# Kernel tuning notes

Measured on AMD Instinct MI355X. Metric: run time of the kernel, lower is better.

## Reference

```python
import jax, jax.numpy as jnp
import numpy as np

B, F, N = 32, 10, 512   # batch_num, win_size (all_feature), node_num
E = 8192                # edges per graph
INTER = 256             # GAT inter_dim
HEADS = 2
NEG_SLOPE = 0.2
BN_EPS = 1e-5


def setup_inputs() -> dict:
    key = jax.random.key(0)
    ks = jax.random.split(key, 16)
    data = jax.random.normal(ks[0], (B, F, N), dtype=jnp.float32)
    # loop-free random edges: src != dst (matches PyG remove_self_loops + add_self_loops)
    dst = jax.random.randint(ks[1], (E,), 0, N)
    off = jax.random.randint(ks[2], (E,), 1, N)
    src = (dst + off) % N
    org_edge_index = jnp.stack([src, dst]).astype(jnp.int64)
    g = 0.05
    return {
        "data": data,
        "org_edge_index": org_edge_index,
        "W1": jax.random.normal(ks[3], (F, HEADS * INTER), dtype=jnp.float32) * g,
        "as1": jax.random.normal(ks[4], (HEADS, INTER), dtype=jnp.float32) * g,
        "ad1": jax.random.normal(ks[5], (HEADS, INTER), dtype=jnp.float32) * g,
        "b1": jnp.zeros((HEADS * INTER,), dtype=jnp.float32),
        "W2": jax.random.normal(ks[6], (HEADS * INTER, HEADS * INTER), dtype=jnp.float32) * g,
        "as2": jax.random.normal(ks[7], (HEADS, INTER), dtype=jnp.float32) * g,
        "ad2": jax.random.normal(ks[8], (HEADS, INTER), dtype=jnp.float32) * g,
        "b2": jnp.zeros((HEADS * INTER,), dtype=jnp.float32),
        "Wfc": jax.random.normal(ks[9], (HEADS * INTER, 1), dtype=jnp.float32) * g,
        "bfc": jnp.zeros((1,), dtype=jnp.float32),
        "gamma": jnp.ones((1,), dtype=jnp.float32),
        "beta": jnp.zeros((1,), dtype=jnp.float32),
    }


def _gat_conv(x, src, dst, W, a_src, a_dst, b):
    # PyG GATConv (v1), concat=True, negative_slope=0.2
    n = x.shape[0]
    H, C = a_src.shape
    h = (x @ W).reshape(n, H, C)                       # [n, H, C]
    al_s = jnp.einsum('nhc,hc->nh', h, a_src)          # [n, H]
    al_d = jnp.einsum('nhc,hc->nh', h, a_dst)
    e = jax.nn.leaky_relu(al_s[src] + al_d[dst], NEG_SLOPE)  # [Etot, H]
    emax = jax.ops.segment_max(e, dst, num_segments=n)       # segment softmax over dst
    ex = jnp.exp(e - emax[dst])
    denom = jax.ops.segment_sum(ex, dst, num_segments=n)
    alpha = ex / (denom[dst] + 1e-16)                  # [Etot, H]
    msg = h[src] * alpha[:, :, None]                   # [Etot, H, C]
    out = jax.ops.segment_sum(msg, dst, num_segments=n)
    return out.reshape(n, H * C) + b


def reference(data, org_edge_index, W1, as1, ad1, b1, W2, as2, ad2, b2,
              Wfc, bfc, gamma, beta):
    b_num, feat, n_num = data.shape
    x = data.reshape(-1, feat)                         # faithful to x.view(-1, all_feature)
    total = b_num * n_num
    # batched edge index: repeat with per-batch node offsets
    offs = jnp.arange(b_num, dtype=org_edge_index.dtype) * n_num
    be = (org_edge_index[:, None, :] + offs[None, :, None]).reshape(2, -1)
    loops = jnp.arange(total, dtype=org_edge_index.dtype)  # add_self_loops
    src = jnp.concatenate([be[0], loops])
    dst = jnp.concatenate([be[1], loops])
    x1 = _gat_conv(x, src, dst, W1, as1, ad1, b1)      # dropout = identity (eval)
    x2 = _gat_conv(x1, src, dst, W2, as2, ad2, b2)
    y = x2 @ Wfc + bfc                                 # [total, 1]
    # BatchNorm1d(1), eval mode: running_mean=0, running_var=1
    y = y * (gamma / jnp.sqrt(1.0 + BN_EPS)) + beta
    y = jax.nn.relu(y)
    return y.reshape(-1, 1, n_num)                     # [B, 1, N]
```

## Files before the change

kernel.cpp:

```cpp
#include <hip/hip_runtime.h>
#include <math.h>

#define B_  32
#define F_  10
#define N_  512
#define E_  8192
#define T_  16384
#define EC_ 8704
#define HC_ 512
#define C_  256

typedef __attribute__((ext_vector_type(8))) short bf16x8;
typedef __attribute__((ext_vector_type(4))) float f32x4;

__device__ __forceinline__ unsigned short f2bf(float f) {
    unsigned int u = __float_as_uint(f);
    u = (u + 0x7fffu + ((u >> 16) & 1u)) >> 16;
    return (unsigned short)u;
}
__device__ __forceinline__ float bf2f(unsigned short b) {
    return __uint_as_float(((unsigned int)b) << 16);
}
__device__ __forceinline__ float dot4(f32x4 a, f32x4 b) {
    f32x4 m = a * b;
    return m[0] + m[1] + m[2] + m[3];
}
__device__ __forceinline__ unsigned int pack2(unsigned short a, unsigned short b) {
    return (unsigned int)a | ((unsigned int)b << 16);
}
__device__ __forceinline__ void bf2x2(unsigned int u, float& f0, float& f1) {
    f0 = __uint_as_float(u << 16);
    f1 = __uint_as_float(u & 0xffff0000u);
}
__device__ __forceinline__ void async_cp16(const void* g, void* l) {
    __builtin_amdgcn_global_load_lds(
        (const __attribute__((address_space(1))) unsigned int*)g,
        (__attribute__((address_space(3))) unsigned int*)l, 16, 0, 0);
}

__device__ __forceinline__ int node_map(int bid, int wid) {
    int x = bid & 7;
    int rest = bid >> 3;
    int batch = x * 4 + (rest >> 7);
    int within = rest & 127;
    return batch * 512 + within * 4 + wid;
}

__global__ __launch_bounds__(256) void gemm1_kernel(
    const float* __restrict__ X, const float* __restrict__ W1,
    const float* __restrict__ a_s, const float* __restrict__ a_d,
    unsigned short* __restrict__ Hs, float* __restrict__ als,
    float* __restrict__ ald, float* __restrict__ als2z,
    float* __restrict__ ald2z,
    const int* __restrict__ eidx, const float* __restrict__ W2,
    int* __restrict__ off0, int* __restrict__ csr0,
    unsigned short* __restrict__ Bhi, unsigned short* __restrict__ Blo) {
    __shared__ float shmem[1056];
    int tid = threadIdx.x;

    if (blockIdx.x >= 512) {
        if (blockIdx.x < 768) {
            int pb = blockIdx.x - 512;
            float* t = shmem;
            int bx = pb & 15, by = pb >> 4;
            int kb = bx * 32, nb = by * 32;
            int tx = tid & 31, ty = tid >> 5;
#pragma unroll
            for (int r = ty; r < 32; r += 8)
                t[r * 33 + tx] = W2[(size_t)(kb + r) * HC_ + nb + tx];
            __syncthreads();
#pragma unroll
            for (int r = ty; r < 32; r += 8) {
                float v = t[tx * 33 + r];
                unsigned short h = f2bf(v);
                Bhi[(size_t)(nb + r) * HC_ + kb + tx] = h;
                Blo[(size_t)(nb + r) * HC_ + kb + tx] = f2bf(v - bf2f(h));
            }
        } else {
            int* cnt = (int*)shmem;
            int* scn = (int*)shmem + 512;
            cnt[2 * tid] = 0; cnt[2 * tid + 1] = 0;
            __syncthreads();
            const int* edst = eidx + E_;
            for (int j = tid; j < EC_; j += 256) {
                int d = (j < E_) ? edst[j] : (j - E_);
                atomicAdd(&cnt[d], 1);
            }
            __syncthreads();
            int c0 = cnt[2 * tid], c1 = cnt[2 * tid + 1];
            scn[tid] = c0 + c1;
            __syncthreads();
            for (int d = 1; d < 256; d <<= 1) {
                int add = (tid >= d) ? scn[tid - d] : 0;
                __syncthreads();
                scn[tid] += add;
                __syncthreads();
            }
            int e0 = scn[tid] - (c0 + c1);
            off0[2 * tid] = e0;
            off0[2 * tid + 1] = e0 + c0;
            cnt[2 * tid] = e0;
            cnt[2 * tid + 1] = e0 + c0;
            if (tid == 255) off0[512] = EC_;
            __syncthreads();
            for (int j = tid; j < EC_; j += 256) {
                int s, d;
                if (j < E_) { s = eidx[j]; d = edst[j]; }
                else { s = d = j - E_; }
                int pos = atomicAdd(&cnt[d], 1);
                csr0[pos] = s;
            }
        }
        return;
    }

    float* xs = shmem;
    int lane = tid & 63, w = tid >> 6;
    int q = blockIdx.x;
    int batch = (q & 7) * 4 + (q >> 7);
    int sub = (q >> 3) & 15;
    int nb = batch * 512 + sub * 32 + w * 8;
    int col = lane * 8;

    f32x4 w1r[F_][2];
#pragma unroll
    for (int k = 0; k < F_; ++k) {
        w1r[k][0] = *(const f32x4*)&W1[k * HC_ + col];
        w1r[k][1] = *(const f32x4*)&W1[k * HC_ + col + 4];
    }
    f32x4 asl = *(const f32x4*)&a_s[col], ash = *(const f32x4*)&a_s[col + 4];
    f32x4 adl = *(const f32x4*)&a_d[col], adh = *(const f32x4*)&a_d[col + 4];

    const float* xp = X + (size_t)nb * F_;
    if (lane < 40) {
        xs[w * 80 + lane] = xp[lane];
        xs[w * 80 + lane + 40] = xp[lane + 40];
    }
    if (lane < 16) als2z[nb * 2 + lane] = 0.f;
    else if (lane >= 48) ald2z[nb * 2 + lane - 48] = 0.f;

#pragma unroll
    for (int n = 0; n < 8; ++n) {
        f32x4 h0 = {0.f, 0.f, 0.f, 0.f}, h1 = h0;
#pragma unroll
        for (int k = 0; k < F_; ++k) {
            float xv = xs[w * 80 + n * F_ + k];
            h0 += xv * w1r[k][0];
            h1 += xv * w1r[k][1];
        }
        int node = nb + n;
        uint4 uh;
        uh.x = pack2(f2bf(h0[0]), f2bf(h0[1]));
        uh.y = pack2(f2bf(h0[2]), f2bf(h0[3]));
        uh.z = pack2(f2bf(h1[0]), f2bf(h1[1]));
        uh.w = pack2(f2bf(h1[2]), f2bf(h1[3]));
        *(uint4*)&Hs[(size_t)node * HC_ + col] = uh;
        float ps = dot4(h0, asl) + dot4(h1, ash);
        float pd = dot4(h0, adl) + dot4(h1, adh);
#pragma unroll
        for (int m = 1; m <= 16; m <<= 1) {
            ps += __shfl_xor(ps, m);
            pd += __shfl_xor(pd, m);
        }
        if (lane == 0)  { als[node * 2 + 0] = ps; ald[node * 2 + 0] = pd; }
        if (lane == 32) { als[node * 2 + 1] = ps; ald[node * 2 + 1] = pd; }
    }
}

template <int MODE>
__global__ __launch_bounds__(256) void agg_kernel(
    const unsigned short* __restrict__ Hin, const float* __restrict__ als,
    const float* __restrict__ ald, const int* __restrict__ off0,
    const int* __restrict__ csr0, const float* __restrict__ bias,
    unsigned short* __restrict__ Ahi,
    const float* __restrict__ Wfc, const float* __restrict__ bfc,
    const float* __restrict__ gamma, const float* __restrict__ beta,
    float* __restrict__ out) {
    int tid = threadIdx.x, lane = tid & 63, wid = tid >> 6;
    int dst = node_map(blockIdx.x, wid);
    int bbase = dst & ~511;
    int dl = dst & 511;
    int beg = off0[dl], end = off0[dl + 1], deg = end - beg;
    float ad0 = ald[2 * dst], ad1 = ald[2 * dst + 1];
    int col = lane * 8;
    float A[8] = {0.f, 0.f, 0.f, 0.f, 0.f, 0.f, 0.f, 0.f};

    if (deg <= 64) {
        float e0 = -1e30f, e1 = -1e30f;
        int sl = 0;
        if (lane < deg) {
            sl = csr0[beg + lane] + bbase;
            float a0 = als[2 * sl], a1 = als[2 * sl + 1];
            e0 = a0 + ad0; e0 = e0 > 0.f ? e0 : 0.2f * e0;
            e1 = a1 + ad1; e1 = e1 > 0.f ? e1 : 0.2f * e1;
        }
        float m0 = e0, m1 = e1;
#pragma unroll
        for (int m = 1; m < 64; m <<= 1) {
            m0 = fmaxf(m0, __shfl_xor(m0, m));
            m1 = fmaxf(m1, __shfl_xor(m1, m));
        }
        float x0 = (lane < deg) ? expf(e0 - m0) : 0.f;
        float x1 = (lane < deg) ? expf(e1 - m1) : 0.f;
        float d0 = x0, d1 = x1;
#pragma unroll
        for (int m = 1; m < 64; m <<= 1) {
            d0 += __shfl_xor(d0, m);
            d1 += __shfl_xor(d1, m);
        }
        float w0l = x0 / (d0 + 1e-16f);
        float w1l = x1 / (d1 + 1e-16f);
        int e = 0;
        for (; e + 4 <= deg; e += 4) {
            int s0 = __shfl(sl, e), s1 = __shfl(sl, e + 1);
            int s2 = __shfl(sl, e + 2), s3 = __shfl(sl, e + 3);
            float wa0 = __shfl(w0l, e),     wb0 = __shfl(w1l, e);
            float wa1 = __shfl(w0l, e + 1), wb1 = __shfl(w1l, e + 1);
            float wa2 = __shfl(w0l, e + 2), wb2 = __shfl(w1l, e + 2);
            float wa3 = __shfl(w0l, e + 3), wb3 = __shfl(w1l, e + 3);
            float w0 = (lane < 32) ? wa0 : wb0;
            float w1 = (lane < 32) ? wa1 : wb1;
            float w2 = (lane < 32) ? wa2 : wb2;
            float w3 = (lane < 32) ? wa3 : wb3;
            uint4 h0 = *(const uint4*)(Hin + (size_t)s0 * HC_ + col);
            uint4 h1 = *(const uint4*)(Hin + (size_t)s1 * HC_ + col);
            uint4 h2 = *(const uint4*)(Hin + (size_t)s2 * HC_ + col);
            uint4 h3 = *(const uint4*)(Hin + (size_t)s3 * HC_ + col);
            float f0, f1;
            bf2x2(h0.x, f0, f1); A[0] = fmaf(w0, f0, A[0]); A[1] = fmaf(w0, f1, A[1]);
            bf2x2(h0.y, f0, f1); A[2] = fmaf(w0, f0, A[2]); A[3] = fmaf(w0, f1, A[3]);
            bf2x2(h0.z, f0, f1); A[4] = fmaf(w0, f0, A[4]); A[5] = fmaf(w0, f1, A[5]);
            bf2x2(h0.w, f0, f1); A[6] = fmaf(w0, f0, A[6]); A[7] = fmaf(w0, f1, A[7]);
            bf2x2(h1.x, f0, f1); A[0] = fmaf(w1, f0, A[0]); A[1] = fmaf(w1, f1, A[1]);
            bf2x2(h1.y, f0, f1); A[2] = fmaf(w1, f0, A[2]); A[3] = fmaf(w1, f1, A[3]);
            bf2x2(h1.z, f0, f1); A[4] = fmaf(w1, f0, A[4]); A[5] = fmaf(w1, f1, A[5]);
            bf2x2(h1.w, f0, f1); A[6] = fmaf(w1, f0, A[6]); A[7] = fmaf(w1, f1, A[7]);
            bf2x2(h2.x, f0, f1); A[0] = fmaf(w2, f0, A[0]); A[1] = fmaf(w2, f1, A[1]);
            bf2x2(h2.y, f0, f1); A[2] = fmaf(w2, f0, A[2]); A[3] = fmaf(w2, f1, A[3]);
            bf2x2(h2.z, f0, f1); A[4] = fmaf(w2, f0, A[4]); A[5] = fmaf(w2, f1, A[5]);
            bf2x2(h2.w, f0, f1); A[6] = fmaf(w2, f0, A[6]); A[7] = fmaf(w2, f1, A[7]);
            bf2x2(h3.x, f0, f1); A[0] = fmaf(w3, f0, A[0]); A[1] = fmaf(w3, f1, A[1]);
            bf2x2(h3.y, f0, f1); A[2] = fmaf(w3, f0, A[2]); A[3] = fmaf(w3, f1, A[3]);
            bf2x2(h3.z, f0, f1); A[4] = fmaf(w3, f0, A[4]); A[5] = fmaf(w3, f1, A[5]);
            bf2x2(h3.w, f0, f1); A[6] = fmaf(w3, f0, A[6]); A[7] = fmaf(w3, f1, A[7]);
        }
        for (; e < deg; ++e) {
            int s = __shfl(sl, e);
            float wa = __shfl(w0l, e);
            float wb = __shfl(w1l, e);
            float w = (lane < 32) ? wa : wb;
            uint4 hv = *(const uint4*)(Hin + (size_t)s * HC_ + col);
            float f0, f1;
            bf2x2(hv.x, f0, f1); A[0] = fmaf(w, f0, A[0]); A[1] = fmaf(w, f1, A[1]);
            bf2x2(hv.y, f0, f1); A[2] = fmaf(w, f0, A[2]); A[3] = fmaf(w, f1, A[3]);
            bf2x2(hv.z, f0, f1); A[4] = fmaf(w, f0, A[4]); A[5] = fmaf(w, f1, A[5]);
            bf2x2(hv.w, f0, f1); A[6] = fmaf(w, f0, A[6]); A[7] = fmaf(w, f1, A[7]);
        }
    } else {
        float m0 = -1e30f, m1 = -1e30f;
        for (int k = beg + lane; k < end; k += 64) {
            int s = csr0[k] + bbase;
            float e0 = als[2 * s] + ad0; e0 = e0 > 0.f ? e0 : 0.2f * e0;
            float e1 = als[2 * s + 1] + ad1; e1 = e1 > 0.f ? e1 : 0.2f * e1;
            m0 = fmaxf(m0, e0);
            m1 = fmaxf(m1, e1);
        }
#pragma unroll
        for (int m = 1; m < 64; m <<= 1) {
            m0 = fmaxf(m0, __shfl_xor(m0, m));
            m1 = fmaxf(m1, __shfl_xor(m1, m));
        }
        float d0 = 0.f, d1 = 0.f;
        for (int k = beg + lane; k < end; k += 64) {
            int s = csr0[k] + bbase;
            float e0 = als[2 * s] + ad0; e0 = e0 > 0.f ? e0 : 0.2f * e0;
            float e1 = als[2 * s + 1] + ad1; e1 = e1 > 0.f ? e1 : 0.2f * e1;
            d0 += expf(e0 - m0);
            d1 += expf(e1 - m1);
        }
#pragma unroll
        for (int m = 1; m < 64; m <<= 1) {
            d0 += __shfl_xor(d0, m);
            d1 += __shfl_xor(d1, m);
        }
        float inv0 = 1.f / (d0 + 1e-16f);
        float inv1 = 1.f / (d1 + 1e-16f);
        for (int k = beg; k < end; ++k) {
            int s = csr0[k] + bbase;
            float e0 = als[2 * s] + ad0; e0 = e0 > 0.f ? e0 : 0.2f * e0;
            float e1 = als[2 * s + 1] + ad1; e1 = e1 > 0.f ? e1 : 0.2f * e1;
            float w0 = expf(e0 - m0) * inv0;
            float w1 = expf(e1 - m1) * inv1;
            float w = (lane < 32) ? w0 : w1;
            uint4 hv = *(const uint4*)(Hin + (size_t)s * HC_ + col);
            float f0, f1;
            bf2x2(hv.x, f0, f1); A[0] = fmaf(w, f0, A[0]); A[1] = fmaf(w, f1, A[1]);
            bf2x2(hv.y, f0, f1); A[2] = fmaf(w, f0, A[2]); A[3] = fmaf(w, f1, A[3]);
            bf2x2(hv.z, f0, f1); A[4] = fmaf(w, f0, A[4]); A[5] = fmaf(w, f1, A[5]);
            bf2x2(hv.w, f0, f1); A[6] = fmaf(w, f0, A[6]); A[7] = fmaf(w, f1, A[7]);
        }
    }

#pragma unroll
    for (int j = 0; j < 8; ++j) A[j] += bias[col + j];

    if (MODE == 0) {
        uint4 uh;
        uh.x = pack2(f2bf(A[0]), f2bf(A[1]));
        uh.y = pack2(f2bf(A[2]), f2bf(A[3]));
        uh.z = pack2(f2bf(A[4]), f2bf(A[5]));
        uh.w = pack2(f2bf(A[6]), f2bf(A[7]));
        *(uint4*)&Ahi[(size_t)dst * HC_ + col] = uh;
    } else {
        float y = 0.f;
#pragma unroll
        for (int j = 0; j < 8; ++j) y = fmaf(A[j], Wfc[col + j], y);
#pragma unroll
        for (int m = 1; m < 64; m <<= 1) y += __shfl_xor(y, m);
        if (lane == 0) {
            y += bfc[0];
            y = y * (gamma[0] * rsqrtf(1.f + 1e-5f)) + beta[0];
            out[dst] = y > 0.f ? y : 0.f;
        }
    }
}

__global__ __launch_bounds__(512, 1) void gemm2_kernel(
    const unsigned short* __restrict__ Ahi,
    const unsigned short* __restrict__ Bhi, const unsigned short* __restrict__ Blo,
    unsigned short* __restrict__ H2,
    const float* __restrict__ as2, const float* __restrict__ ad2,
    float* __restrict__ als2, float* __restrict__ ald2) {
    __shared__ __align__(16) char smem[135168];
    const int tid = threadIdx.x, lane = tid & 63, wid = tid >> 6;
    const int wr = wid >> 1, wc = wid & 1;
    const int g = (blockIdx.x & 7) * 32 + (blockIdx.x >> 3);
    const int row0 = (g >> 2) * 256, col0 = (g & 3) * 128;
    const int lr = lane & 15, lk = lane >> 4;
    const int x7 = lr & 7;

    f32x4 acc[4][4] = {};

    const char* gsrc[8];
    int loff[8];
#pragma unroll
    for (int l = 0; l < 8; ++l) {
        int i = tid + l * 512;
        if (i < 2048) {
            int r = i >> 3, c = i & 7;
            gsrc[l] = (const char*)(Ahi + (size_t)(row0 + r) * HC_ + ((c ^ (r & 7)) << 3));
            loff[l] = i << 4;
        } else if (i < 3072) {
            int j = i - 2048, r = j >> 3, c = j & 7;
            gsrc[l] = (const char*)(Bhi + (size_t)(col0 + r) * HC_ + ((c ^ (r & 7)) << 3));
            loff[l] = 32768 + (j << 4);
        } else {
            int j = i - 3072, r = j >> 3, c = j & 7;
            gsrc[l] = (const char*)(Blo + (size_t)(col0 + r) * HC_ + ((c ^ (r & 7)) << 3));
            loff[l] = 49152 + (j << 4);
        }
    }
    char* lds0 = smem;

#pragma unroll
    for (int l = 0; l < 8; ++l) async_cp16(gsrc[l], lds0 + loff[l]);
    asm volatile("s_waitcnt vmcnt(0)" ::: "memory");
    __builtin_amdgcn_s_barrier();

    int cur = 0;
    for (int kt = 0; kt < 8; ++kt) {
        if (kt < 7) {
            char* dst = lds0 + ((cur ^ 1) << 16);
#pragma unroll
            for (int l = 0; l < 8; ++l)
                async_cp16(gsrc[l] + (size_t)(kt + 1) * 128, dst + loff[l]);
        }
        const char* base = lds0 + (cur << 16);
#pragma unroll
        for (int kk = 0; kk < 2; ++kk) {
            bf16x8 a[4], bh[4], bl[4];
            int cx = ((kk * 4 + lk) ^ x7) << 4;
#pragma unroll
            for (int m = 0; m < 4; ++m) {
                int ra = wr * 64 + m * 16 + lr;
                int rb = wc * 64 + m * 16 + lr;
                a[m]  = *(const bf16x8*)(base + ra * 128 + cx);
                bh[m] = *(const bf16x8*)(base + 32768 + rb * 128 + cx);
                bl[m] = *(const bf16x8*)(base + 49152 + rb * 128 + cx);
            }
#pragma unroll
            for (int m = 0; m < 4; ++m)
#pragma unroll
                for (int n = 0; n < 4; ++n) {
                    acc[m][n] = __builtin_amdgcn_mfma_f32_16x16x32_bf16(a[m], bh[n], acc[m][n], 0, 0, 0);
                    acc[m][n] = __builtin_amdgcn_mfma_f32_16x16x32_bf16(a[m], bl[n], acc[m][n], 0, 0, 0);
                }
        }
        asm volatile("s_waitcnt vmcnt(0)" ::: "memory");
        __builtin_amdgcn_s_barrier();
        cur ^= 1;
    }

    float* tb = (float*)smem;
#pragma unroll
    for (int m = 0; m < 4; ++m)
#pragma unroll
        for (int i = 0; i < 4; ++i) {
            int row = wr * 64 + m * 16 + lk * 4 + i;
#pragma unroll
            for (int n = 0; n < 4; ++n)
                tb[row * 132 + wc * 64 + n * 16 + lr] = acc[m][n][i];
        }
    __syncthreads();
    const int head = col0 >> 8;
    const float* a_s2 = as2 + head * C_ + (col0 & 255);
    const float* a_d2 = ad2 + head * C_ + (col0 & 255);
#pragma unroll
    for (int p = 0; p < 8; ++p) {
        int q = tid + p * 512;
        int row = q >> 4, cs = (q & 15) * 8;
        const float* v = &tb[row * 132 + cs];
        uint4 uh;
        uh.x = pack2(f2bf(v[0]), f2bf(v[1]));
        uh.y = pack2(f2bf(v[2]), f2bf(v[3]));
        uh.z = pack2(f2bf(v[4]), f2bf(v[5]));
        uh.w = pack2(f2bf(v[6]), f2bf(v[7]));
        *(uint4*)&H2[(size_t)(row0 + row) * HC_ + col0 + cs] = uh;
        float ps = 0.f, pd = 0.f;
#pragma unroll
        for (int j = 0; j < 8; ++j) {
            ps = fmaf(v[j], a_s2[cs + j], ps);
            pd = fmaf(v[j], a_d2[cs + j], pd);
        }
#pragma unroll
        for (int m = 1; m < 16; m <<= 1) {
            ps += __shfl_xor(ps, m);
            pd += __shfl_xor(pd, m);
        }
        if ((tid & 15) == 0) {
            atomicAdd(&als2[(row0 + row) * 2 + head], ps);
            atomicAdd(&ald2[(row0 + row) * 2 + head], pd);
        }
    }
}

extern "C" void kernel_launch(void* const* d_in, const int* in_sizes, int n_in,
                              void* d_out, int out_size, void* d_ws, size_t ws_size,
                              hipStream_t stream) {
    const float* data  = (const float*)d_in[0];
    const int*   eidx  = (const int*)d_in[1];
    const float* W1    = (const float*)d_in[2];
    const float* as1   = (const float*)d_in[3];
    const float* ad1   = (const float*)d_in[4];
    const float* b1    = (const float*)d_in[5];
    const float* W2    = (const float*)d_in[6];
    const float* as2   = (const float*)d_in[7];
    const float* ad2   = (const float*)d_in[8];
    const float* b2    = (const float*)d_in[9];
    const float* Wfc   = (const float*)d_in[10];
    const float* bfc   = (const float*)d_in[11];
    const float* gamma = (const float*)d_in[12];
    const float* beta  = (const float*)d_in[13];
    float* out = (float*)d_out;

    char* base = (char*)d_ws;
    size_t o = 0;
    auto take = [&](size_t bytes) {
        char* p = base + o;
        o = (o + bytes + 255) & ~(size_t)255;
        return p;
    };
    int*   off0 = (int*)take((size_t)(N_ + 1) * 4);
    int*   csr0 = (int*)take((size_t)EC_ * 4);
    float* als1 = (float*)take((size_t)T_ * 2 * 4);
    float* ald1 = (float*)take((size_t)T_ * 2 * 4);
    float* als2 = (float*)take((size_t)T_ * 2 * 4);
    float* ald2 = (float*)take((size_t)T_ * 2 * 4);
    unsigned short* hs1 = (unsigned short*)take((size_t)T_ * HC_ * 2);
    unsigned short* hs2 = (unsigned short*)take((size_t)T_ * HC_ * 2);
    unsigned short* Ahi = (unsigned short*)take((size_t)T_ * HC_ * 2);
    unsigned short* Bhi = (unsigned short*)take((size_t)HC_ * HC_ * 2);
    unsigned short* Blo = (unsigned short*)take((size_t)HC_ * HC_ * 2);

    gemm1_kernel<<<769, 256, 0, stream>>>(data, W1, as1, ad1, hs1, als1, ald1,
                                          als2, ald2, eidx, W2, off0, csr0,
                                          Bhi, Blo);
    agg_kernel<0><<<4096, 256, 0, stream>>>(hs1, als1, ald1, off0, csr0, b1,
                                            Ahi, nullptr, nullptr, nullptr,
                                            nullptr, nullptr);
    gemm2_kernel<<<256, 512, 0, stream>>>(Ahi, Bhi, Blo, hs2, as2, ad2, als2, ald2);
    agg_kernel<1><<<4096, 256, 0, stream>>>(hs2, als2, ald2, off0, csr0, b2,
                                            nullptr, Wfc, bfc, gamma,
                                            beta, out);
}
```

Measured before the change: 92.78 us.

## Shrink gemm2 tiles to 128x128 with 256 threads and K-step 32

The second-layer GEMM drops from 256x128 tiles with 512 threads and one block per CU to 128x128 tiles with 256 threads, 512 blocks and two blocks per CU. The K step shrinks from 64 to 32, so there are 16 double-buffered iterations with a new 4-column XOR swizzle and LDS use is halved. The aim is better CU occupancy and load balance across the GPU, since 256 blocks barely cover the CUs. In exchange, B-matrix data is reused less and there are twice as many barriers.

```diff
diff --git a/kernel.cpp b/kernel.cpp
--- a/kernel.cpp
+++ b/kernel.cpp
@@ -325,77 +325,68 @@
     }
 }
 
-__global__ __launch_bounds__(512, 1) void gemm2_kernel(
+__global__ __launch_bounds__(256, 2) void gemm2_kernel(
     const unsigned short* __restrict__ Ahi,
     const unsigned short* __restrict__ Bhi, const unsigned short* __restrict__ Blo,
     unsigned short* __restrict__ H2,
     const float* __restrict__ as2, const float* __restrict__ ad2,
     float* __restrict__ als2, float* __restrict__ ald2) {
-    __shared__ __align__(16) char smem[135168];
+    __shared__ __align__(16) char smem[67584];
     const int tid = threadIdx.x, lane = tid & 63, wid = tid >> 6;
     const int wr = wid >> 1, wc = wid & 1;
-    const int g = (blockIdx.x & 7) * 32 + (blockIdx.x >> 3);
-    const int row0 = (g >> 2) * 256, col0 = (g & 3) * 128;
+    const int g = (blockIdx.x & 7) * 64 + (blockIdx.x >> 3);
+    const int row0 = (g >> 2) * 128, col0 = (g & 3) * 128;
     const int lr = lane & 15, lk = lane >> 4;
-    const int x7 = lr & 7;
+    const int cswz = (lk ^ ((lr >> 1) & 3)) << 4;
 
     f32x4 acc[4][4] = {};
 
-    const char* gsrc[8];
-    int loff[8];
-#pragma unroll
-    for (int l = 0; l < 8; ++l) {
-        int i = tid + l * 512;
-        if (i < 2048) {
-            int r = i >> 3, c = i & 7;
-            gsrc[l] = (const char*)(Ahi + (size_t)(row0 + r) * HC_ + ((c ^ (r & 7)) << 3));
-            loff[l] = i << 4;
-        } else if (i < 3072) {
-            int j = i - 2048, r = j >> 3, c = j & 7;
-            gsrc[l] = (const char*)(Bhi + (size_t)(col0 + r) * HC_ + ((c ^ (r & 7)) << 3));
-            loff[l] = 32768 + (j << 4);
-        } else {
-            int j = i - 3072, r = j >> 3, c = j & 7;
-            gsrc[l] = (const char*)(Blo + (size_t)(col0 + r) * HC_ + ((c ^ (r & 7)) << 3));
-            loff[l] = 49152 + (j << 4);
-        }
-    }
-    char* lds0 = smem;
-
-#pragma unroll
-    for (int l = 0; l < 8; ++l) async_cp16(gsrc[l], lds0 + loff[l]);
+    const char* gsrc[6];
+    int loff[6];
+#pragma unroll
+    for (int l = 0; l < 6; ++l) {
+        int i = tid + l * 256;
+        int mat = i >> 9;
+        int j = i & 511;
+        int r = j >> 2, c = j & 3;
+        int cs = c ^ ((r >> 1) & 3);
+        const unsigned short* bp = (mat == 0) ? (Ahi + (size_t)(row0 + r) * HC_)
+                               : (mat == 1) ? (Bhi + (size_t)(col0 + r) * HC_)
+                                            : (Blo + (size_t)(col0 + r) * HC_);
+        gsrc[l] = (const char*)(bp + cs * 8);
+        loff[l] = mat * 8192 + j * 16;
+    }
+
+#pragma unroll
+    for (int l = 0; l < 6; ++l) async_cp16(gsrc[l], smem + loff[l]);
     asm volatile("s_waitcnt vmcnt(0)" ::: "memory");
     __builtin_amdgcn_s_barrier();
 
     int cur = 0;
-    for (int kt = 0; kt < 8; ++kt) {
-        if (kt < 7) {
-            char* dst = lds0 + ((cur ^ 1) << 16);
-#pragma unroll
-            for (int l = 0; l < 8; ++l)
-                async_cp16(gsrc[l] + (size_t)(kt + 1) * 128, dst + loff[l]);
-        }
-        const char* base = lds0 + (cur << 16);
-#pragma unroll
-        for (int kk = 0; kk < 2; ++kk) {
-            bf16x8 a[4], bh[4], bl[4];
-            int cx = ((kk * 4 + lk) ^ x7) << 4;
-#pragma unroll
-            for (int m = 0; m < 4; ++m) {
-                int ra = wr * 64 + m * 16 + lr;
-                int rb = wc * 64 + m * 16 + lr;
-                a[m]  = *(const bf16x8*)(base + ra * 128 + cx);
-                bh[m] = *(const bf16x8*)(base + 32768 + rb * 128 + cx);
-                bl[m] = *(const bf16x8*)(base + 49152 + rb * 128 + cx);
+    for (int kt = 0; kt < 16; ++kt) {
+        if (kt < 15) {
+            char* dst = smem + (cur ^ 1) * 24576;
+#pragma unroll
+            for (int l = 0; l < 6; ++l)
+                async_cp16(gsrc[l] + (size_t)(kt + 1) * 64, dst + loff[l]);
+        }
+        const char* base = smem + cur * 24576;
+        bf16x8 a[4], bh[4], bl[4];
+#pragma unroll
+        for (int m = 0; m < 4; ++m) {
+            int ra = wr * 64 + m * 16 + lr;
+            int rb = wc * 64 + m * 16 + lr;
+            a[m]  = *(const bf16x8*)(base + ra * 64 + cswz);
+            bh[m] = *(const bf16x8*)(base + 8192 + rb * 64 + cswz);
+            bl[m] = *(const bf16x8*)(base + 16384 + rb * 64 + cswz);
+        }
+#pragma unroll
+        for (int m = 0; m < 4; ++m)
+#pragma unroll
+            for (int n = 0; n < 4; ++n) {
+                acc[m][n] = __builtin_amdgcn_mfma_f32_16x16x32_bf16(a[m], bh[n], acc[m][n], 0, 0, 0);
+                acc[m][n] = __builtin_amdgcn_mfma_f32_16x16x32_bf16(a[m], bl[n], acc[m][n], 0, 0, 0);
             }
-#pragma unroll
-            for (int m = 0; m < 4; ++m)
-#pragma unroll
-                for (int n = 0; n < 4; ++n) {
-                    acc[m][n] = __builtin_amdgcn_mfma_f32_16x16x32_bf16(a[m], bh[n], acc[m][n], 0, 0, 0);
-                    acc[m][n] = __builtin_amdgcn_mfma_f32_16x16x32_bf16(a[m], bl[n], acc[m][n], 0, 0, 0);
-                }
-        }
         asm volatile("s_waitcnt vmcnt(0)" ::: "memory");
         __builtin_amdgcn_s_barrier();
         cur ^= 1;
@@ -417,7 +408,7 @@
     const float* a_d2 = ad2 + head * C_ + (col0 & 255);
 #pragma unroll
     for (int p = 0; p < 8; ++p) {
-        int q = tid + p * 512;
+        int q = tid + p * 256;
         int row = q >> 4, cs = (q & 15) * 8;
         const float* v = &tb[row * 132 + cs];
         uint4 uh;
@@ -488,7 +479,7 @@
     agg_kernel<0><<<4096, 256, 0, stream>>>(hs1, als1, ald1, off0, csr0, b1,
                                             Ahi, nullptr, nullptr, nullptr,
                                             nullptr, nullptr);
-    gemm2_kernel<<<256, 512, 0, stream>>>(Ahi, Bhi, Blo, hs2, as2, ad2, als2, ald2);
+    gemm2_kernel<<<512, 256, 0, stream>>>(Ahi, Bhi, Blo, hs2, as2, ad2, als2, ald2);
     agg_kernel<1><<<4096, 256, 0, stream>>>(hs2, als2, ald2, off0, csr0, b2,
                                             nullptr, Wfc, bfc, gamma,
                                             beta, out);
```

New measurement: 94.41 us. No clear change (+1.8%).
